# Optimization experiments

Measured on AMD Instinct MI355X. Metric: run time of the kernel, lower is better.

The kernel has to match this reference:

```python
import jax, jax.numpy as jnp
import numpy as np
from jax import lax

D_MODEL = 256
D_STATE = 16
BATCH = 4
SEQ = 16384
LN_EPS = 1e-5


def setup_inputs() -> dict:
    key = jax.random.key(0)
    ks = jax.random.split(key, 16)
    d, s = D_MODEL, D_STATE
    lim = 1.0 / np.sqrt(d)
    u = lambda k, shape, l: jax.random.uniform(k, shape, jnp.float32, -l, l)
    return {
        "x": jax.random.normal(ks[0], (BATCH, SEQ, d), jnp.float32),
        # forward branch params (torch Linear stored as (in, out))
        "W_fproj": u(ks[1], (d, 2 * d), lim),
        "b_fproj": u(ks[2], (2 * d,), lim),
        "A_f": jax.random.normal(ks[3], (s, d), jnp.float32),
        "W_fgate": u(ks[4], (d, s), lim),
        "b_fgate": u(ks[5], (s,), lim),
        # backward branch params
        "W_bproj": u(ks[6], (d, 2 * d), lim),
        "b_bproj": u(ks[7], (2 * d,), lim),
        "A_b": jax.random.normal(ks[8], (s, d), jnp.float32),
        "W_bgate": u(ks[9], (d, s), lim),
        "b_bgate": u(ks[10], (s,), lim),
        # output proj + layernorm
        "W_out": u(ks[11], (2 * d, d), 1.0 / np.sqrt(2 * d)),
        "b_out": u(ks[12], (d,), 1.0 / np.sqrt(2 * d)),
        "ln_g": jnp.ones((d,), jnp.float32),
        "ln_b": jnp.zeros((d,), jnp.float32),
    }


def _scan_dir(x, W_proj, b_proj, A, W_gate, b_gate):
    """One direction: gated state-space scan. x: (B,S,D) -> (B,S,D)."""
    B, S, D = x.shape
    proj = x @ W_proj + b_proj            # (B,S,2D)
    value = proj[..., D:]                 # the 'gate' chunk is unused in the original
    gw = jax.nn.sigmoid(value @ W_gate + b_gate)  # (B,S,d_state)

    def step(state, inp):
        g, v = inp                        # g:(B,Ns), v:(B,D)
        gi = g[:, :, None]                # (B,Ns,1)
        upd = A[None, :, :] * v[:, None, :]
        state = state * gi + upd * (1.0 - gi)
        out = (state * gi).sum(axis=1)    # (B,D)
        return state, out

    init = jnp.zeros((B, A.shape[0], D), x.dtype)
    _, outs = lax.scan(step, init, (gw.transpose(1, 0, 2), value.transpose(1, 0, 2)))
    return outs.transpose(1, 0, 2)        # (B,S,D)


def reference(x, W_fproj, b_fproj, A_f, W_fgate, b_fgate,
              W_bproj, b_bproj, A_b, W_bgate, b_bgate,
              W_out, b_out, ln_g, ln_b):
    fwd = _scan_dir(x, W_fproj, b_fproj, A_f, W_fgate, b_fgate)
    x_rev = jnp.flip(x, axis=1)
    bwd = jnp.flip(_scan_dir(x_rev, W_bproj, b_bproj, A_b, W_bgate, b_bgate), axis=1)
    combined = jnp.concatenate([fwd, bwd], axis=-1)    # (B,S,2D)
    out = combined @ W_out + b_out                     # (B,S,D)
    mu = out.mean(axis=-1, keepdims=True)
    var = out.var(axis=-1, keepdims=True)
    out = (out - mu) * lax.rsqrt(var + LN_EPS) * ln_g + ln_b
    return out  # dropout is identity in eval mode
```

## Files before the change

kernel.cpp:

```cpp
#include <hip/hip_runtime.h>

#define SEQ   16384
#define NB    4
#define NROWS 65536
#define NC    512
#define CL    32

typedef short bf16x8 __attribute__((ext_vector_type(8)));
typedef float f32x4  __attribute__((ext_vector_type(4)));
typedef float f32x2  __attribute__((ext_vector_type(2)));

__device__ inline float bf2f(ushort u) {
    unsigned int t = ((unsigned int)u) << 16;
    float f; __builtin_memcpy(&f, &t, 4); return f;
}
__device__ inline float bflo(uint u) {
    uint t = u << 16; float f; __builtin_memcpy(&f, &t, 4); return f;
}
__device__ inline float bfhi(uint u) {
    uint t = u & 0xffff0000u; float f; __builtin_memcpy(&f, &t, 4); return f;
}
__device__ inline ushort f2bf(float f) {
    unsigned int b; __builtin_memcpy(&b, &f, 4);
    unsigned int r = (b + 0x7FFFu + ((b >> 16) & 1u)) >> 16;
    return (ushort)r;
}

__device__ inline f32x2 pk_fma(f32x2 a, f32x2 b, f32x2 c) {
    f32x2 d;
    asm("v_pk_fma_f32 %0, %1, %2, %3" : "=v"(d) : "v"(a), "v"(b), "v"(c));
    return d;
}
__device__ inline f32x2 pk_mul(f32x2 a, f32x2 b) {
    f32x2 d;
    asm("v_pk_mul_f32 %0, %1, %2" : "=v"(d) : "v"(a), "v"(b));
    return d;
}
__device__ inline f32x2 pk_sub(f32x2 a, f32x2 b) {
    f32x2 d;
    asm("v_pk_add_f32 %0, %1, %2 neg_lo:[0,1] neg_hi:[0,1]" : "=v"(d) : "v"(a), "v"(b));
    return d;
}

__global__ __launch_bounds__(256) void prep_weights(
    const float* __restrict__ Wf, const float* __restrict__ Wb,
    const float* __restrict__ Wo, const float* __restrict__ Wgf,
    const float* __restrict__ Wgb, const float* __restrict__ bfp,
    const float* __restrict__ bbp, const float* __restrict__ A_f,
    const float* __restrict__ A_b,
    ushort* __restrict__ BTv, ushort* __restrict__ WoT,
    ushort* __restrict__ WgT, float* __restrict__ bias_v,
    float* __restrict__ AsT)
{
    int idx = blockIdx.x * 256 + threadIdx.x;
    if (idx < 131072) {
        int dir = idx >> 16, j = idx & 65535, n = j >> 8, k = j & 255;
        const float* W = dir ? Wb : Wf;
        BTv[idx] = f2bf(W[k * 512 + 256 + n]);
    } else if (idx < 262144) {
        int j = idx - 131072; int n = j >> 9, k = j & 511;
        WoT[j] = f2bf(Wo[k * 256 + n]);
    } else if (idx < 270336) {
        int j = idx - 262144; int dir = j >> 12, jj = j & 4095, s = jj >> 8, k = jj & 255;
        WgT[j] = f2bf((dir ? Wgb : Wgf)[k * 16 + s]);
    } else if (idx < 270848) {
        int j = idx - 270336; int dir = j >> 8, n = j & 255;
        bias_v[j] = (dir ? bbp : bfp)[256 + n];
    } else if (idx < 279040) {
        int j = idx - 270848; int dir = j >> 12, jj = j & 4095, d = jj >> 4, s = jj & 15;
        AsT[j] = (dir ? A_b : A_f)[s * 256 + d];
    }
}

__global__ __launch_bounds__(512) void gemm_value(
    const float* __restrict__ x, const ushort* __restrict__ BTv,
    const float* __restrict__ bias_v, ushort* __restrict__ value)
{
    __shared__ ushort Al[128 * 40];
    __shared__ ushort Bl[256 * 40];
    const int tid = threadIdx.x;
    const int m0 = blockIdx.y * 128, dir = blockIdx.x;
    const ushort* BT = BTv + dir * 65536;
    const int w = tid >> 6, l = tid & 63;
    const int wr = w >> 2, wc = w & 3;
    const int l15 = l & 15, lk = (l >> 4) * 8;
    f32x4 acc[4][4] = {};

    for (int kk = 0; kk < 256; kk += 32) {
        {
            int r = tid >> 2, c = (tid & 3) * 8;
            const float* xp = x + (size_t)(m0 + r) * 256 + kk + c;
            float4 a = *(const float4*)xp;
            float4 b = *(const float4*)(xp + 4);
            ushort u[8];
            u[0] = f2bf(a.x); u[1] = f2bf(a.y); u[2] = f2bf(a.z); u[3] = f2bf(a.w);
            u[4] = f2bf(b.x); u[5] = f2bf(b.y); u[6] = f2bf(b.z); u[7] = f2bf(b.w);
            *(uint4*)&Al[r * 40 + c] = *(uint4*)u;
        }
        #pragma unroll
        for (int i = 0; i < 2; ++i) {
            int idx = tid + i * 512; int r = idx >> 2, c = idx & 3;
            *(uint4*)&Bl[r * 40 + c * 8] = *(const uint4*)(BT + (size_t)r * 256 + kk + c * 8);
        }
        __syncthreads();
        bf16x8 af[4], bfr[4];
        #pragma unroll
        for (int m = 0; m < 4; ++m) af[m] = *(const bf16x8*)&Al[(wr * 64 + m * 16 + l15) * 40 + lk];
        #pragma unroll
        for (int n = 0; n < 4; ++n) bfr[n] = *(const bf16x8*)&Bl[(wc * 64 + n * 16 + l15) * 40 + lk];
        #pragma unroll
        for (int m = 0; m < 4; ++m)
            #pragma unroll
            for (int n = 0; n < 4; ++n)
                acc[m][n] = __builtin_amdgcn_mfma_f32_16x16x32_bf16(af[m], bfr[n], acc[m][n], 0, 0, 0);
        __syncthreads();
    }
    const int rbase = (l >> 4) * 4;
    #pragma unroll
    for (int m = 0; m < 4; ++m)
        #pragma unroll
        for (int n = 0; n < 4; ++n) {
            int col = wc * 64 + n * 16 + l15;
            float bv = bias_v[dir * 256 + col];
            #pragma unroll
            for (int r = 0; r < 4; ++r) {
                int row = m0 + wr * 64 + m * 16 + rbase + r;
                value[(size_t)row * 512 + dir * 256 + col] = f2bf(acc[m][n][r] + bv);
            }
        }
}

__global__ __launch_bounds__(256) void gate_scan(
    const ushort* __restrict__ value, const ushort* __restrict__ WgT,
    const float* __restrict__ bgf, const float* __restrict__ bgb,
    float* __restrict__ gw, ushort* __restrict__ L16, float* __restrict__ P)
{
    __shared__ ushort Av[64 * 264];
    __shared__ float gsm[64 * 16];
    const int tid = threadIdx.x;
    const int r0 = blockIdx.x * 64, dir = blockIdx.y;
    #pragma unroll
    for (int i = 0; i < 8; ++i) {
        int idx = tid + i * 256; int r = idx >> 5, c = idx & 31;
        *(uint4*)&Av[r * 264 + c * 8] =
            *(const uint4*)(value + (size_t)(r0 + r) * 512 + dir * 256 + c * 8);
    }
    __syncthreads();
    const int w = tid >> 6, l = tid & 63, l15 = l & 15, lk = (l >> 4) * 8;
    const ushort* Wg = WgT + dir * 4096;
    f32x4 acc = {};
    #pragma unroll
    for (int kk = 0; kk < 256; kk += 32) {
        bf16x8 af = *(const bf16x8*)&Av[(w * 16 + l15) * 264 + kk + lk];
        bf16x8 bf = *(const bf16x8*)(Wg + l15 * 256 + kk + lk);
        acc = __builtin_amdgcn_mfma_f32_16x16x32_bf16(af, bf, acc, 0, 0, 0);
    }
    const float bgs = (dir ? bgb : bgf)[l15];
    const int rbase = (l >> 4) * 4;
    const int b = r0 >> 14, t0 = r0 & 16383;
    #pragma unroll
    for (int r = 0; r < 4; ++r) {
        int lr = w * 16 + rbase + r;
        float sv = 1.f / (1.f + __expf(-(acc[r] + bgs)));
        gsm[lr * 16 + l15] = sv;
        gw[((size_t)(dir * NB + b) * SEQ + t0 + lr) * 16 + l15] = sv;
    }
    __syncthreads();
    const int d = tid;
    #pragma unroll
    for (int ci = 0; ci < 2; ++ci) {
        const int chunk = (t0 >> 5) + ci;
        f32x2 c[8] = {};
        for (int i = 0; i < CL; ++i) {
            int row = dir ? (CL - 1 - i) : i;
            float v = bf2f(Av[(ci * 32 + row) * 264 + d]);
            f32x2 vd = {v, v};
            #pragma unroll
            for (int sp = 0; sp < 8; ++sp) {
                f32x2 g = *(const f32x2*)&gsm[(ci * 32 + row) * 16 + sp * 2];
                c[sp] = pk_fma(g, pk_sub(c[sp], vd), vd);
            }
        }
        ushort ub[16];
        #pragma unroll
        for (int sp = 0; sp < 8; ++sp) {
            ub[2 * sp]     = f2bf(c[sp].x);
            ub[2 * sp + 1] = f2bf(c[sp].y);
        }
        ushort* Lp = L16 + ((size_t)(dir * NB + b) * NC + chunk) * 4096 + d * 16;
        *(uint4*)Lp       = *(uint4*)&ub[0];
        *(uint4*)(Lp + 8) = *(uint4*)&ub[8];
    }
    if (tid < 32) {
        int ci2 = tid >> 4, s = tid & 15;
        float p = 1.f;
        for (int t = 0; t < CL; ++t) p *= gsm[(ci2 * 32 + t) * 16 + s];
        P[((size_t)(dir * NB + b) * NC + (t0 >> 5) + ci2) * 16 + s] = p;
    }
}

__global__ __launch_bounds__(256, 2) void chunk_scan(
    ushort* __restrict__ L16, const float* __restrict__ P)
{
    const int bid = blockIdx.x;
    const int dir = bid >> 6, b = (bid >> 4) & 3, dgrp = bid & 15;
    const int tid = threadIdx.x;
    const int s = tid & 15;
    const size_t cb = (size_t)(dir * NB + b) * NC;
    ushort* Lb = L16 + cb * 4096 + dgrp * 256 + tid;
    const float* Pb = P + cb * 16 + s;
    float e = 0.f;
    ushort lA[16], lB[16];
    float pA[16], pB[16];

#define LOADB(la, pa, ib) { _Pragma("unroll") \
    for (int j = 0; j < 16; ++j) { \
        int t = (ib) * 16 + j; int k = dir ? (NC - 1 - t) : t; \
        la[j] = Lb[(size_t)k * 4096]; pa[j] = Pb[k * 16]; } }
#define PROCB(la, pa, ib) { _Pragma("unroll") \
    for (int j = 0; j < 16; ++j) { \
        int t = (ib) * 16 + j; int k = dir ? (NC - 1 - t) : t; \
        Lb[(size_t)k * 4096] = f2bf(e); e = pa[j] * e + bf2f(la[j]); } }

    LOADB(lA, pA, 0)
    for (int ib = 0; ib < 32; ib += 2) {
        LOADB(lB, pB, ib + 1)
        PROCB(lA, pA, ib)
        if (ib + 2 < 32) { LOADB(lA, pA, ib + 2) }
        PROCB(lB, pB, ib + 1)
    }
#undef LOADB
#undef PROCB
}

__global__ __launch_bounds__(256) void pass_c(
    ushort* __restrict__ value, const float* __restrict__ gw,
    const ushort* __restrict__ L16, const float* __restrict__ AsT)
{
    const int chunk = blockIdx.x, b = blockIdx.y, dir = blockIdx.z;
    const int tid = threadIdx.x;
    __shared__ float gs[CL * 16];
    __shared__ ushort vs[CL * 256];
    const float* gwd = gw + ((size_t)(dir * NB + b) * SEQ + chunk * CL) * 16;
    if (tid < 128) ((float4*)gs)[tid] = ((const float4*)gwd)[tid];
    ushort* vg = value + ((size_t)b * SEQ + chunk * CL) * 512 + dir * 256;
    #pragma unroll
    for (int i = 0; i < 4; ++i) {
        int idx = tid + i * 256;
        int r = idx >> 5, cc = idx & 31;
        *(uint4*)&vs[r * 256 + cc * 8] = *(const uint4*)(vg + (size_t)r * 512 + cc * 8);
    }
    __syncthreads();
    const int d = tid;
    const float* Ad = AsT + dir * 4096 + d * 16;
    const ushort* Lp = L16 + ((size_t)(dir * NB + b) * NC + chunk) * 4096 + d * 16;
    f32x2 a[8], c[8];
    #pragma unroll
    for (int sp = 0; sp < 8; ++sp) {
        a[sp] = *(const f32x2*)(Ad + sp * 2);
        uint u = *(const uint*)(Lp + sp * 2);
        c[sp].x = bflo(u); c[sp].y = bfhi(u);
    }
    for (int i = 0; i < CL; ++i) {
        int row = dir ? (CL - 1 - i) : i;
        float v = bf2f(vs[row * 256 + d]);
        f32x2 vd = {v, v};
        f32x2 o = {0.f, 0.f};
        #pragma unroll
        for (int sp = 0; sp < 8; ++sp) {
            f32x2 g = *(const f32x2*)&gs[row * 16 + sp * 2];
            c[sp] = pk_fma(g, pk_sub(c[sp], vd), vd);
            o = pk_fma(a[sp], pk_mul(g, c[sp]), o);
        }
        vs[row * 256 + d] = f2bf(o.x + o.y);
    }
    __syncthreads();
    #pragma unroll
    for (int i = 0; i < 4; ++i) {
        int idx = tid + i * 256;
        int r = idx >> 5, cc = idx & 31;
        *(uint4*)(vg + (size_t)r * 512 + cc * 8) = *(uint4*)&vs[r * 256 + cc * 8];
    }
}

__global__ __launch_bounds__(512) void gemm_out_ln(
    const ushort* __restrict__ A, const ushort* __restrict__ BT,
    const float* __restrict__ b_out, const float* __restrict__ ln_g,
    const float* __restrict__ ln_b, float* __restrict__ out)
{
    __shared__ ushort Al[128 * 40];
    __shared__ ushort Bl[256 * 40];
    __shared__ float red[2][2][4][64];
    const int tid = threadIdx.x;
    const int m0 = blockIdx.x * 128;
    const int w = tid >> 6, l = tid & 63;
    const int wr = w >> 2, wc = w & 3;
    const int l15 = l & 15, lk = (l >> 4) * 8;
    f32x4 acc[4][4] = {};

    for (int kk = 0; kk < 512; kk += 32) {
        {
            int r = tid >> 2, c = tid & 3;
            *(uint4*)&Al[r * 40 + c * 8] = *(const uint4*)(A + (size_t)(m0 + r) * 512 + kk + c * 8);
        }
        #pragma unroll
        for (int i = 0; i < 2; ++i) {
            int idx = tid + i * 512; int r = idx >> 2, c = idx & 3;
            *(uint4*)&Bl[r * 40 + c * 8] = *(const uint4*)(BT + (size_t)r * 512 + kk + c * 8);
        }
        __syncthreads();
        bf16x8 af[4], bfr[4];
        #pragma unroll
        for (int m = 0; m < 4; ++m) af[m] = *(const bf16x8*)&Al[(wr * 64 + m * 16 + l15) * 40 + lk];
        #pragma unroll
        for (int n = 0; n < 4; ++n) bfr[n] = *(const bf16x8*)&Bl[(wc * 64 + n * 16 + l15) * 40 + lk];
        #pragma unroll
        for (int m = 0; m < 4; ++m)
            #pragma unroll
            for (int n = 0; n < 4; ++n)
                acc[m][n] = __builtin_amdgcn_mfma_f32_16x16x32_bf16(af[m], bfr[n], acc[m][n], 0, 0, 0);
        __syncthreads();
    }
    const int rbase = (l >> 4) * 4;
    float gg[4], bb[4];
    #pragma unroll
    for (int n = 0; n < 4; ++n) {
        int col = wc * 64 + n * 16 + l15;
        float bv = b_out[col];
        gg[n] = ln_g[col]; bb[n] = ln_b[col];
        #pragma unroll
        for (int m = 0; m < 4; ++m)
            #pragma unroll
            for (int r = 0; r < 4; ++r)
                acc[m][n][r] += bv;
    }
    float s1[4][4], s2[4][4];
    #pragma unroll
    for (int m = 0; m < 4; ++m)
        #pragma unroll
        for (int r = 0; r < 4; ++r) {
            float a_ = 0.f, b_ = 0.f;
            #pragma unroll
            for (int n = 0; n < 4; ++n) {
                float v = acc[m][n][r];
                a_ += v; b_ += v * v;
            }
            s1[m][r] = a_; s2[m][r] = b_;
        }
    #pragma unroll
    for (int mask = 1; mask < 16; mask <<= 1)
        #pragma unroll
        for (int m = 0; m < 4; ++m)
            #pragma unroll
            for (int r = 0; r < 4; ++r) {
                s1[m][r] += __shfl_xor(s1[m][r], mask, 64);
                s2[m][r] += __shfl_xor(s2[m][r], mask, 64);
            }
    if (l15 == 0) {
        #pragma unroll
        for (int m = 0; m < 4; ++m)
            #pragma unroll
            for (int r = 0; r < 4; ++r) {
                int row = m * 16 + rbase + r;
                red[0][wr][wc][row] = s1[m][r];
                red[1][wr][wc][row] = s2[m][r];
            }
    }
    __syncthreads();
    #pragma unroll
    for (int m = 0; m < 4; ++m)
        #pragma unroll
        for (int r = 0; r < 4; ++r) {
            int row = m * 16 + rbase + r;
            float t1 = red[0][wr][0][row] + red[0][wr][1][row] + red[0][wr][2][row] + red[0][wr][3][row];
            float t2 = red[1][wr][0][row] + red[1][wr][1][row] + red[1][wr][2][row] + red[1][wr][3][row];
            float mu = t1 * (1.f / 256.f);
            float var = t2 * (1.f / 256.f) - mu * mu;
            float rs = rsqrtf(var + 1e-5f);
            #pragma unroll
            for (int n = 0; n < 4; ++n) {
                int col = wc * 64 + n * 16 + l15;
                out[(size_t)(m0 + wr * 64 + row) * 256 + col] = (acc[m][n][r] - mu) * rs * gg[n] + bb[n];
            }
        }
}

extern "C" void kernel_launch(void* const* d_in, const int* in_sizes, int n_in,
                              void* d_out, int out_size, void* d_ws, size_t ws_size,
                              hipStream_t stream)
{
    const float* x       = (const float*)d_in[0];
    const float* W_fproj = (const float*)d_in[1];
    const float* b_fproj = (const float*)d_in[2];
    const float* A_f     = (const float*)d_in[3];
    const float* W_fgate = (const float*)d_in[4];
    const float* b_fgate = (const float*)d_in[5];
    const float* W_bproj = (const float*)d_in[6];
    const float* b_bproj = (const float*)d_in[7];
    const float* A_b     = (const float*)d_in[8];
    const float* W_bgate = (const float*)d_in[9];
    const float* b_bgate = (const float*)d_in[10];
    const float* W_out   = (const float*)d_in[11];
    const float* b_out   = (const float*)d_in[12];
    const float* ln_g    = (const float*)d_in[13];
    const float* ln_b    = (const float*)d_in[14];

    char* ws = (char*)d_ws;
    ushort* value  = (ushort*)(ws + 0);
    float*  gw     = (float*) (ws + 67108864);
    ushort* L16    = (ushort*)(ws + 75497472);
    float*  P      = (float*) (ws + 109051904);
    ushort* BTv    = (ushort*)(ws + 109314048);
    ushort* WoT    = (ushort*)(ws + 109576192);
    ushort* WgT    = (ushort*)(ws + 109838336);
    float*  bias_v = (float*) (ws + 109854720);
    float*  AsT    = (float*) (ws + 109856768);

    prep_weights<<<1090, 256, 0, stream>>>(W_fproj, W_bproj, W_out, W_fgate, W_bgate,
                                           b_fproj, b_bproj, A_f, A_b,
                                           BTv, WoT, WgT, bias_v, AsT);
    gemm_value<<<dim3(2, 512), 512, 0, stream>>>(x, BTv, bias_v, value);
    gate_scan<<<dim3(1024, 2), 256, 0, stream>>>(value, WgT, b_fgate, b_bgate, gw, L16, P);
    chunk_scan<<<128, 256, 0, stream>>>(L16, P);
    pass_c<<<dim3(NC, NB, 2), 256, 0, stream>>>(value, gw, L16, AsT);
    gemm_out_ln<<<512, 512, 0, stream>>>(value, WoT, b_out, ln_g, ln_b, (float*)d_out);
}
```

Before: 210.4 us.

## Compute local scan outputs in gate_scan and apply carry as linear correction

gate_scan now computes the zero-init in-chunk scan output (A-weighted gated state sum) and writes it back into value. It also stores per-step cumulative gate products q = g*prefix(g) in place of the raw gates. pass_c no longer reruns the sequential recurrence; it adds the carried-in state contribution as a dot product of q with A*carry for each row. This moves the per-chunk recurrence work out of pass_c at the cost of an extra value write in gate_scan and a launch-bounds occupancy hint.

```diff
diff --git a/kernel.cpp b/kernel.cpp
--- a/kernel.cpp
+++ b/kernel.cpp
@@ -130,10 +130,11 @@
         }
 }
 
-__global__ __launch_bounds__(256) void gate_scan(
-    const ushort* __restrict__ value, const ushort* __restrict__ WgT,
+__global__ __launch_bounds__(256, 4) void gate_scan(
+    ushort* __restrict__ value, const ushort* __restrict__ WgT,
     const float* __restrict__ bgf, const float* __restrict__ bgb,
-    float* __restrict__ gw, ushort* __restrict__ L16, float* __restrict__ P)
+    float* __restrict__ qg, ushort* __restrict__ L16, float* __restrict__ P,
+    const float* __restrict__ AsT)
 {
     __shared__ ushort Av[64 * 264];
     __shared__ float gsm[64 * 16];
@@ -163,10 +164,25 @@
         int lr = w * 16 + rbase + r;
         float sv = 1.f / (1.f + __expf(-(acc[r] + bgs)));
         gsm[lr * 16 + l15] = sv;
-        gw[((size_t)(dir * NB + b) * SEQ + t0 + lr) * 16 + l15] = sv;
-    }
-    __syncthreads();
+    }
+    __syncthreads();
+    if (tid < 32) {
+        int ci = tid >> 4, s = tid & 15;
+        float pfx = 1.f;
+        float* qb = qg + ((size_t)(dir * NB + b) * SEQ + t0 + ci * 32) * 16 + s;
+        for (int i = 0; i < CL; ++i) {
+            int r = dir ? (CL - 1 - i) : i;
+            float g = gsm[(ci * 32 + r) * 16 + s];
+            pfx *= g;
+            qb[r * 16] = g * pfx;
+        }
+        P[((size_t)(dir * NB + b) * NC + (t0 >> 5) + ci) * 16 + s] = pfx;
+    }
     const int d = tid;
+    const float* Ad = AsT + dir * 4096 + d * 16;
+    f32x2 a[8];
+    #pragma unroll
+    for (int sp = 0; sp < 8; ++sp) a[sp] = *(const f32x2*)(Ad + sp * 2);
     #pragma unroll
     for (int ci = 0; ci < 2; ++ci) {
         const int chunk = (t0 >> 5) + ci;
@@ -175,11 +191,14 @@
             int row = dir ? (CL - 1 - i) : i;
             float v = bf2f(Av[(ci * 32 + row) * 264 + d]);
             f32x2 vd = {v, v};
+            f32x2 o = {0.f, 0.f};
             #pragma unroll
             for (int sp = 0; sp < 8; ++sp) {
                 f32x2 g = *(const f32x2*)&gsm[(ci * 32 + row) * 16 + sp * 2];
                 c[sp] = pk_fma(g, pk_sub(c[sp], vd), vd);
-            }
+                o = pk_fma(a[sp], pk_mul(g, c[sp]), o);
+            }
+            Av[(ci * 32 + row) * 264 + d] = f2bf(o.x + o.y);
         }
         ushort ub[16];
         #pragma unroll
@@ -191,11 +210,12 @@
         *(uint4*)Lp       = *(uint4*)&ub[0];
         *(uint4*)(Lp + 8) = *(uint4*)&ub[8];
     }
-    if (tid < 32) {
-        int ci2 = tid >> 4, s = tid & 15;
-        float p = 1.f;
-        for (int t = 0; t < CL; ++t) p *= gsm[(ci2 * 32 + t) * 16 + s];
-        P[((size_t)(dir * NB + b) * NC + (t0 >> 5) + ci2) * 16 + s] = p;
+    __syncthreads();
+    #pragma unroll
+    for (int i = 0; i < 8; ++i) {
+        int idx = tid + i * 256; int r = idx >> 5, c = idx & 31;
+        *(uint4*)(value + (size_t)(r0 + r) * 512 + dir * 256 + c * 8) =
+            *(uint4*)&Av[r * 264 + c * 8];
     }
 }
 
@@ -234,15 +254,15 @@
 }
 
 __global__ __launch_bounds__(256) void pass_c(
-    ushort* __restrict__ value, const float* __restrict__ gw,
+    ushort* __restrict__ value, const float* __restrict__ qg,
     const ushort* __restrict__ L16, const float* __restrict__ AsT)
 {
     const int chunk = blockIdx.x, b = blockIdx.y, dir = blockIdx.z;
     const int tid = threadIdx.x;
-    __shared__ float gs[CL * 16];
+    __shared__ float qs[CL * 16];
     __shared__ ushort vs[CL * 256];
-    const float* gwd = gw + ((size_t)(dir * NB + b) * SEQ + chunk * CL) * 16;
-    if (tid < 128) ((float4*)gs)[tid] = ((const float4*)gwd)[tid];
+    const float* qd = qg + ((size_t)(dir * NB + b) * SEQ + chunk * CL) * 16;
+    if (tid < 128) ((float4*)qs)[tid] = ((const float4*)qd)[tid];
     ushort* vg = value + ((size_t)b * SEQ + chunk * CL) * 512 + dir * 256;
     #pragma unroll
     for (int i = 0; i < 4; ++i) {
@@ -250,29 +270,27 @@
         int r = idx >> 5, cc = idx & 31;
         *(uint4*)&vs[r * 256 + cc * 8] = *(const uint4*)(vg + (size_t)r * 512 + cc * 8);
     }
-    __syncthreads();
     const int d = tid;
     const float* Ad = AsT + dir * 4096 + d * 16;
     const ushort* Lp = L16 + ((size_t)(dir * NB + b) * NC + chunk) * 4096 + d * 16;
-    f32x2 a[8], c[8];
+    f32x2 h[8];
     #pragma unroll
     for (int sp = 0; sp < 8; ++sp) {
-        a[sp] = *(const f32x2*)(Ad + sp * 2);
+        f32x2 a = *(const f32x2*)(Ad + sp * 2);
         uint u = *(const uint*)(Lp + sp * 2);
-        c[sp].x = bflo(u); c[sp].y = bfhi(u);
-    }
-    for (int i = 0; i < CL; ++i) {
-        int row = dir ? (CL - 1 - i) : i;
-        float v = bf2f(vs[row * 256 + d]);
-        f32x2 vd = {v, v};
-        f32x2 o = {0.f, 0.f};
+        f32x2 E; E.x = bflo(u); E.y = bfhi(u);
+        h[sp] = pk_mul(a, E);
+    }
+    __syncthreads();
+    for (int row = 0; row < CL; ++row) {
+        f32x2 corr = {0.f, 0.f};
         #pragma unroll
         for (int sp = 0; sp < 8; ++sp) {
-            f32x2 g = *(const f32x2*)&gs[row * 16 + sp * 2];
-            c[sp] = pk_fma(g, pk_sub(c[sp], vd), vd);
-            o = pk_fma(a[sp], pk_mul(g, c[sp]), o);
-        }
-        vs[row * 256 + d] = f2bf(o.x + o.y);
+            f32x2 q = *(const f32x2*)&qs[row * 16 + sp * 2];
+            corr = pk_fma(q, h[sp], corr);
+        }
+        float outv = bf2f(vs[row * 256 + d]) + corr.x + corr.y;
+        vs[row * 256 + d] = f2bf(outv);
     }
     __syncthreads();
     #pragma unroll
@@ -407,7 +425,7 @@
 
     char* ws = (char*)d_ws;
     ushort* value  = (ushort*)(ws + 0);
-    float*  gw     = (float*) (ws + 67108864);
+    float*  qg     = (float*) (ws + 67108864);
     ushort* L16    = (ushort*)(ws + 75497472);
     float*  P      = (float*) (ws + 109051904);
     ushort* BTv    = (ushort*)(ws + 109314048);
@@ -420,8 +438,8 @@
                                            b_fproj, b_bproj, A_f, A_b,
                                            BTv, WoT, WgT, bias_v, AsT);
     gemm_value<<<dim3(2, 512), 512, 0, stream>>>(x, BTv, bias_v, value);
-    gate_scan<<<dim3(1024, 2), 256, 0, stream>>>(value, WgT, b_fgate, b_bgate, gw, L16, P);
+    gate_scan<<<dim3(1024, 2), 256, 0, stream>>>(value, WgT, b_fgate, b_bgate, qg, L16, P, AsT);
     chunk_scan<<<128, 256, 0, stream>>>(L16, P);
-    pass_c<<<dim3(NC, NB, 2), 256, 0, stream>>>(value, gw, L16, AsT);
+    pass_c<<<dim3(NC, NB, 2), 256, 0, stream>>>(value, qg, L16, AsT);
     gemm_out_ln<<<512, 512, 0, stream>>>(value, WoT, b_out, ln_g, ln_b, (float*)d_out);
 }
```

Result: slower. 219.0 us (+4.1%).
